# Kernel tuning notes

Hardware: AMD Instinct MI355X
Metric: run time of the kernel (lower is better)

The kernel has to match this reference:

```python
import jax, jax.numpy as jnp
import numpy as np
import math

B, Q_LEN, K_LEN = 8, 512, 512
D_MODEL, H = 512, 8
DK = D_MODEL // H


def setup_inputs() -> dict:
    key = jax.random.key(0)
    ks = jax.random.split(key, 12)
    inp = {
        "query": jax.random.normal(ks[0], (B, Q_LEN, D_MODEL), jnp.float32),
        "key": jax.random.normal(ks[1], (B, K_LEN, D_MODEL), jnp.float32),
        "value": jax.random.normal(ks[2], (B, K_LEN, D_MODEL), jnp.float32),
        "relative_embeddings": jax.random.normal(ks[3], (K_LEN, Q_LEN, D_MODEL), jnp.float32),
        # causal mask: 1 = attend, 0 = masked
        "mask": jnp.tril(jnp.ones((Q_LEN, K_LEN), dtype=bool)),
        "Wq": jax.random.normal(ks[4], (D_MODEL, D_MODEL), jnp.float32) / math.sqrt(D_MODEL),
        "Wk": jax.random.normal(ks[5], (D_MODEL, D_MODEL), jnp.float32) / math.sqrt(D_MODEL),
        "Wv": jax.random.normal(ks[6], (D_MODEL, D_MODEL), jnp.float32) / math.sqrt(D_MODEL),
        "Wo": jax.random.normal(ks[7], (D_MODEL, D_MODEL), jnp.float32) / math.sqrt(D_MODEL),
        "Wr": jax.random.normal(ks[8], (D_MODEL, D_MODEL), jnp.float32) / math.sqrt(D_MODEL),
        "u": jax.random.normal(ks[9], (H, DK), jnp.float32),
        "v": jax.random.normal(ks[10], (H, DK), jnp.float32),
    }
    return inp


def reference(query, key, value, relative_embeddings, mask, Wq, Wk, Wv, Wo, Wr, u, v):
    b, q_len, d_model = query.shape
    k_len = key.shape[1]
    # torch nn.Linear(x) = x @ W.T (bias=False)
    Qh = (query @ Wq.T).reshape(b, q_len, H, DK).transpose(0, 2, 1, 3)   # bhqd
    Kh = (key @ Wk.T).reshape(b, k_len, H, DK).transpose(0, 2, 1, 3)     # bhkd
    Vh = (value @ Wv.T).reshape(b, k_len, H, DK).transpose(0, 2, 1, 3)   # bhkd
    # relative position projection: (k_len, q_len, d_model)
    R = relative_embeddings @ Wr.T
    # view(k,q,H,dk).permute(2,1,0,3) -> (H, q, k, dk)
    Rh = R.reshape(k_len, q_len, H, DK).transpose(2, 1, 0, 3)
    # content score: (Q + u) K^T
    content = jnp.einsum("bhqd,bhkd->bhqk", Qh + u[None, :, None, :], Kh)
    # position score: (Q + v) R^T, R per-head per-query
    position = jnp.einsum("bhqd,hqkd->bhqk", Qh + v[None, :, None, :], Rh)
    scores = (content + position) / math.sqrt(DK)
    scores = jnp.where(mask[None, None, :, :], scores, -1e9)
    weights = jax.nn.softmax(scores, axis=-1)  # dropout is identity in eval
    out = jnp.einsum("bhqk,bhkd->bhqd", weights, Vh)
    out = out.transpose(0, 2, 1, 3).reshape(b, q_len, d_model)
    out = out @ Wo.T
    return (out, weights)
```

## Files before the change

### kernel.cpp

```cpp
#include <hip/hip_runtime.h>

#define BATCH   8
#define SEQ     512
#define DMODEL  512
#define NHEAD   8
#define DKH     64

typedef __attribute__((ext_vector_type(8))) short bf16x8;
typedef __attribute__((ext_vector_type(4))) float f32x4;

__device__ __forceinline__ short f2bf(float f) {
    union { float f; unsigned u; } v; v.f = f;
    unsigned r = v.u + 0x7FFFu + ((v.u >> 16) & 1u);
    return (short)(r >> 16);
}

#define LDK 40

__device__ __forceinline__ void stage_f32(const float* __restrict__ base,
                                          int rstride, short* lds, int tid) {
    int r = tid >> 2, c = (tid & 3) << 3;
    const float* p = base + (size_t)r * rstride + c;
    float4 x = *(const float4*)p;
    float4 y = *(const float4*)(p + 4);
    union { short s[8]; bf16x8 v; } o;
    o.s[0] = f2bf(x.x); o.s[1] = f2bf(x.y); o.s[2] = f2bf(x.z); o.s[3] = f2bf(x.w);
    o.s[4] = f2bf(y.x); o.s[5] = f2bf(y.y); o.s[6] = f2bf(y.z); o.s[7] = f2bf(y.w);
    *(bf16x8*)(lds + r * LDK + c) = o.v;
}

__device__ __forceinline__ void stage_bf16(const short* __restrict__ base,
                                           int rstride, short* lds, int tid) {
    int r = tid >> 2, c = (tid & 3) << 3;
    bf16x8 v = *(const bf16x8*)(base + (size_t)r * rstride + c);
    *(bf16x8*)(lds + r * LDK + c) = v;
}

__device__ __forceinline__ void mma_tile(const short* As, const short* Bs,
                                         int lane, int wm, int wn, f32x4 acc[2][2]) {
    int lo = lane & 15, hi = lane >> 4;
    bf16x8 a0 = *(const bf16x8*)(As + (wm * 32 + lo) * LDK + hi * 8);
    bf16x8 a1 = *(const bf16x8*)(As + (wm * 32 + 16 + lo) * LDK + hi * 8);
    bf16x8 b0 = *(const bf16x8*)(Bs + (wn * 32 + lo) * LDK + hi * 8);
    bf16x8 b1 = *(const bf16x8*)(Bs + (wn * 32 + 16 + lo) * LDK + hi * 8);
    acc[0][0] = __builtin_amdgcn_mfma_f32_16x16x32_bf16(a0, b0, acc[0][0], 0, 0, 0);
    acc[0][1] = __builtin_amdgcn_mfma_f32_16x16x32_bf16(a0, b1, acc[0][1], 0, 0, 0);
    acc[1][0] = __builtin_amdgcn_mfma_f32_16x16x32_bf16(a1, b0, acc[1][0], 0, 0, 0);
    acc[1][1] = __builtin_amdgcn_mfma_f32_16x16x32_bf16(a1, b1, acc[1][1], 0, 0, 0);
}

__global__ __launch_bounds__(256) void qkvw_kernel(
        const float* __restrict__ query, const float* __restrict__ key_,
        const float* __restrict__ value,
        const float* __restrict__ Wq, const float* __restrict__ Wk,
        const float* __restrict__ Wv, const float* __restrict__ Wr,
        const float* __restrict__ uvec, const float* __restrict__ vvec,
        short* __restrict__ Qu, short* __restrict__ Qv,
        short* __restrict__ Kh, short* __restrict__ Vt,
        short* __restrict__ Wrt) {
    __shared__ short As[64 * LDK], Bs[64 * LDK];
    int f = blockIdx.x, tid = threadIdx.x;
    if (f >= 1536) {
        int base = (f - 1536) * 1024;
        #pragma unroll
        for (int j = 0; j < 4; j++) {
            int idx = base + j * 256 + tid;
            int n = idx >> 9, m = idx & 511;
            Wrt[idx] = f2bf(Wr[(size_t)m * 512 + n]);
        }
        return;
    }
    int i = f >> 3;
    int nt = i & 7;
    int gm = (f & 7) * 24 + (i >> 3);
    int mode = gm >> 6, mt = gm & 63;
    const float* x = mode == 0 ? query : (mode == 1 ? key_ : value);
    const float* W = mode == 0 ? Wq : (mode == 1 ? Wk : Wv);
    int lane = tid & 63, w = tid >> 6, wm = w >> 1, wn = w & 1;
    const float* Abase = x + (size_t)mt * 64 * DMODEL;
    const float* Bbase = W + (size_t)nt * 64 * DMODEL;
    f32x4 acc[2][2] = {};
    for (int kt = 0; kt < DMODEL; kt += 32) {
        __syncthreads();
        stage_f32(Abase + kt, DMODEL, As, tid);
        stage_f32(Bbase + kt, DMODEL, Bs, tid);
        __syncthreads();
        mma_tile(As, Bs, lane, wm, wn, acc);
    }
    int lo = lane & 15, hi = lane >> 4;
    for (int fm = 0; fm < 2; fm++)
        for (int fn = 0; fn < 2; fn++)
            for (int r = 0; r < 4; r++) {
                int m = mt * 64 + wm * 32 + fm * 16 + hi * 4 + r;
                int n = nt * 64 + wn * 32 + fn * 16 + lo;
                float val = acc[fm][fn][r];
                int b = m >> 9, s = m & 511, h = n >> 6, d = n & 63;
                if (mode == 0) {
                    size_t idx = ((size_t)(b * NHEAD + h) * SEQ + s) * DKH + d;
                    Qu[idx] = f2bf(val + uvec[n]);
                    Qv[idx] = f2bf(val + vvec[n]);
                } else if (mode == 1) {
                    Kh[((size_t)(b * NHEAD + h) * SEQ + s) * DKH + d] = f2bf(val);
                } else {
                    Vt[((size_t)(b * NHEAD + h) * DKH + d) * SEQ + s] = f2bf(val);
                }
            }
}

__global__ __launch_bounds__(256) void t_kernel(const short* __restrict__ Qv,
                                                const short* __restrict__ Wrt,
                                                short* __restrict__ T2) {
    __shared__ short As[64 * LDK], Bs[64 * LDK];
    int f = blockIdx.x;
    int i = f >> 3;
    int nt = i & 7;
    int mh = (f & 7) * 64 + (i >> 3);
    int mt = mh >> 3, h = mh & 7;
    int tid = threadIdx.x, lane = tid & 63, w = tid >> 6, wm = w >> 1, wn = w & 1;
    int m0 = mt * 64, b = m0 >> 9, q0 = m0 & 511;
    const short* Abase = Qv + ((size_t)(b * NHEAD + h) * SEQ + q0) * DKH;
    const short* Bbase = Wrt + (size_t)nt * 64 * DMODEL + h * DKH;
    f32x4 acc[2][2] = {};
    for (int kt = 0; kt < DKH; kt += 32) {
        __syncthreads();
        stage_bf16(Abase + kt, DKH, As, tid);
        stage_bf16(Bbase + kt, DMODEL, Bs, tid);
        __syncthreads();
        mma_tile(As, Bs, lane, wm, wn, acc);
    }
    int lo = lane & 15, hi = lane >> 4;
    int bh = b * NHEAD + h;
    for (int fm = 0; fm < 2; fm++)
        for (int fn = 0; fn < 2; fn++)
            for (int r = 0; r < 4; r++) {
                int q = q0 + wm * 32 + fm * 16 + hi * 4 + r;
                int n = nt * 64 + wn * 32 + fn * 16 + lo;
                T2[((size_t)q * 64 + bh) * DMODEL + n] = f2bf(acc[fm][fn][r]);
            }
}

__global__ __launch_bounds__(256) void content_kernel(const short* __restrict__ Qu,
                                                      const short* __restrict__ Kh,
                                                      float* __restrict__ scores) {
    int f = blockIdx.x;
    int i = f >> 3;
    int bh = (f & 7) * 8 + (i >> 6);
    int rest = i & 63;
    int kt_ = rest & 7, qt = rest >> 3;
    if (kt_ > qt) return;
    __shared__ short As[64 * LDK], Bs[64 * LDK];
    int tid = threadIdx.x, lane = tid & 63, w = tid >> 6, wm = w >> 1, wn = w & 1;
    const short* Abase = Qu + ((size_t)bh * SEQ + qt * 64) * DKH;
    const short* Bbase = Kh + ((size_t)bh * SEQ + kt_ * 64) * DKH;
    f32x4 acc[2][2] = {};
    for (int kt = 0; kt < DKH; kt += 32) {
        __syncthreads();
        stage_bf16(Abase + kt, DKH, As, tid);
        stage_bf16(Bbase + kt, DKH, Bs, tid);
        __syncthreads();
        mma_tile(As, Bs, lane, wm, wn, acc);
    }
    int lo = lane & 15, hi = lane >> 4;
    for (int fm = 0; fm < 2; fm++)
        for (int fn = 0; fn < 2; fn++)
            for (int r = 0; r < 4; r++) {
                int q = qt * 64 + wm * 32 + fm * 16 + hi * 4 + r;
                int k = kt_ * 64 + wn * 32 + fn * 16 + lo;
                scores[((size_t)bh * SEQ + q) * SEQ + k] = acc[fm][fn][r];
            }
}

__global__ __launch_bounds__(512) void position_kernel(const short* __restrict__ T2,
                                                       const float* __restrict__ rel,
                                                       float* __restrict__ scores) {
    int bk = blockIdx.x;
    int x = bk & 7, idx = bk >> 3;
    int q = (idx >> 1) * 8 + x;
    int half = idx & 1;
    if (half * 256 > q) return;
    __shared__ short Tl[64 * 512];
    int tid = threadIdx.x, w = tid >> 6, lane = tid & 63;
    const short* Tq = T2 + (size_t)q * (64 * DMODEL);
    #pragma unroll
    for (int it = 0; it < 8; ++it) {
        int chunk = it * 512 + tid;
        int r = chunk >> 6, c = chunk & 63;
        bf16x8 v = *(const bf16x8*)(Tq + (size_t)chunk * 8);
        *(bf16x8*)(Tl + r * 512 + (c ^ (r & 7)) * 8) = v;
    }
    __syncthreads();
    int kbase = half * 256 + w * 32;
    if (kbase > q) return;
    int lo = lane & 15, hi = lane >> 4;
    const float* relq = rel + ((size_t)kbase * SEQ + q) * DMODEL;
    f32x4 acc[4][2] = {};
    for (int n = 0; n < DMODEL; n += 32) {
        bf16x8 a[4];
        #pragma unroll
        for (int fm = 0; fm < 4; fm++) {
            int rr = fm * 16 + lo;
            int g = ((n >> 3) + hi) ^ (rr & 7);
            a[fm] = *(const bf16x8*)(Tl + rr * 512 + g * 8);
        }
        bf16x8 bfrag[2];
        #pragma unroll
        for (int fk = 0; fk < 2; fk++) {
            const float* p = relq + (size_t)(fk * 16 + lo) * (SEQ * DMODEL) + n + hi * 8;
            float4 xv = *(const float4*)p;
            float4 yv = *(const float4*)(p + 4);
            union { short s[8]; bf16x8 v; } o;
            o.s[0] = f2bf(xv.x); o.s[1] = f2bf(xv.y); o.s[2] = f2bf(xv.z); o.s[3] = f2bf(xv.w);
            o.s[4] = f2bf(yv.x); o.s[5] = f2bf(yv.y); o.s[6] = f2bf(yv.z); o.s[7] = f2bf(yv.w);
            bfrag[fk] = o.v;
        }
        #pragma unroll
        for (int fm = 0; fm < 4; fm++) {
            acc[fm][0] = __builtin_amdgcn_mfma_f32_16x16x32_bf16(a[fm], bfrag[0], acc[fm][0], 0, 0, 0);
            acc[fm][1] = __builtin_amdgcn_mfma_f32_16x16x32_bf16(a[fm], bfrag[1], acc[fm][1], 0, 0, 0);
        }
    }
    #pragma unroll
    for (int fm = 0; fm < 4; fm++)
        #pragma unroll
        for (int fk = 0; fk < 2; fk++)
            #pragma unroll
            for (int r = 0; r < 4; r++) {
                int bh = fm * 16 + hi * 4 + r;
                int k = kbase + fk * 16 + lo;
                scores[((size_t)bh * SEQ + q) * SEQ + k] += acc[fm][fk][r];
            }
}

__global__ __launch_bounds__(256) void pv_sm_kernel(float* __restrict__ scores,
                                                    const short* __restrict__ Vt,
                                                    short* __restrict__ attn) {
    __shared__ short As[64 * LDK], Bs[64 * LDK];
    int f = blockIdx.x;
    int i = f >> 3;
    int bh = (f & 7) * 8 + (i >> 3);
    int qt = i & 7;
    int tid = threadIdx.x, lane = tid & 63, w = tid >> 6, wm = w >> 1, wn = w & 1;
    int kmax = (qt + 1) * 64;
    int r = tid >> 2, c4 = tid & 3;
    int q = qt * 64 + r;
    float* row = scores + ((size_t)bh * SEQ + q) * SEQ;
    float M = -1e30f, S = 0.f;
    int kbeg = c4 * 128;
    int kend = (kbeg + 128 < kmax) ? kbeg + 128 : kmax;
    for (int k = kbeg; k < kend; k += 4) {
        float4 vv = *(const float4*)(row + k);
        float x0 = (k + 0 <= q) ? vv.x * 0.125f : -1e30f;
        float x1 = (k + 1 <= q) ? vv.y * 0.125f : -1e30f;
        float x2 = (k + 2 <= q) ? vv.z * 0.125f : -1e30f;
        float x3 = (k + 3 <= q) ? vv.w * 0.125f : -1e30f;
        float mx = fmaxf(fmaxf(x0, x1), fmaxf(x2, x3));
        float Mn = fmaxf(M, mx);
        S = S * __expf(M - Mn) + __expf(x0 - Mn) + __expf(x1 - Mn)
          + __expf(x2 - Mn) + __expf(x3 - Mn);
        M = Mn;
    }
    #pragma unroll
    for (int off = 1; off <= 2; off <<= 1) {
        float Mo = __shfl_xor(M, off), So = __shfl_xor(S, off);
        float Mn = fmaxf(M, Mo);
        S = S * __expf(M - Mn) + So * __expf(Mo - Mn);
        M = Mn;
    }
    float invS = 1.0f / S;
    const short* Bbase = Vt + (size_t)bh * DKH * SEQ;
    f32x4 acc[2][2] = {};
    int cc = c4 * 8;
    for (int kt = 0; kt < SEQ; kt += 32) {
        if (kt < kmax) {
            __syncthreads();
            stage_bf16(Bbase + kt, SEQ, Bs, tid);
            float4 x = *(const float4*)(row + kt + cc);
            float4 y = *(const float4*)(row + kt + cc + 4);
            float p0 = (kt + cc + 0 <= q) ? __expf(x.x * 0.125f - M) * invS : 0.f;
            float p1 = (kt + cc + 1 <= q) ? __expf(x.y * 0.125f - M) * invS : 0.f;
            float p2 = (kt + cc + 2 <= q) ? __expf(x.z * 0.125f - M) * invS : 0.f;
            float p3 = (kt + cc + 3 <= q) ? __expf(x.w * 0.125f - M) * invS : 0.f;
            float p4 = (kt + cc + 4 <= q) ? __expf(y.x * 0.125f - M) * invS : 0.f;
            float p5 = (kt + cc + 5 <= q) ? __expf(y.y * 0.125f - M) * invS : 0.f;
            float p6 = (kt + cc + 6 <= q) ? __expf(y.z * 0.125f - M) * invS : 0.f;
            float p7 = (kt + cc + 7 <= q) ? __expf(y.w * 0.125f - M) * invS : 0.f;
            *(float4*)(row + kt + cc) = make_float4(p0, p1, p2, p3);
            *(float4*)(row + kt + cc + 4) = make_float4(p4, p5, p6, p7);
            union { short s[8]; bf16x8 v; } o;
            o.s[0] = f2bf(p0); o.s[1] = f2bf(p1); o.s[2] = f2bf(p2); o.s[3] = f2bf(p3);
            o.s[4] = f2bf(p4); o.s[5] = f2bf(p5); o.s[6] = f2bf(p6); o.s[7] = f2bf(p7);
            *(bf16x8*)(As + r * LDK + cc) = o.v;
            __syncthreads();
            mma_tile(As, Bs, lane, wm, wn, acc);
        } else {
            float4 z = make_float4(0.f, 0.f, 0.f, 0.f);
            *(float4*)(row + kt + cc) = z;
            *(float4*)(row + kt + cc + 4) = z;
        }
    }
    int lo = lane & 15, hi = lane >> 4;
    int b = bh >> 3, h = bh & 7;
    for (int fm = 0; fm < 2; fm++)
        for (int fn = 0; fn < 2; fn++)
            for (int rr = 0; rr < 4; rr++) {
                int qq = qt * 64 + wm * 32 + fm * 16 + hi * 4 + rr;
                int d = wn * 32 + fn * 16 + lo;
                attn[((size_t)b * SEQ + qq) * DMODEL + h * DKH + d] = f2bf(acc[fm][fn][rr]);
            }
}

__global__ __launch_bounds__(256) void oproj_kernel(const short* __restrict__ attn,
                                                    const float* __restrict__ Wo,
                                                    float* __restrict__ out) {
    __shared__ short As[64 * LDK], Bs[64 * LDK];
    int f = blockIdx.x;
    int i = f >> 3;
    int mt = (f & 7) * 8 + (i >> 3);
    int nt = i & 7;
    int tid = threadIdx.x, lane = tid & 63, w = tid >> 6, wm = w >> 1, wn = w & 1;
    const short* Abase = attn + (size_t)mt * 64 * DMODEL;
    const float* Bbase = Wo + (size_t)nt * 64 * DMODEL;
    f32x4 acc[2][2] = {};
    for (int kt = 0; kt < DMODEL; kt += 32) {
        __syncthreads();
        stage_bf16(Abase + kt, DMODEL, As, tid);
        stage_f32(Bbase + kt, DMODEL, Bs, tid);
        __syncthreads();
        mma_tile(As, Bs, lane, wm, wn, acc);
    }
    int lo = lane & 15, hi = lane >> 4;
    for (int fm = 0; fm < 2; fm++)
        for (int fn = 0; fn < 2; fn++)
            for (int r = 0; r < 4; r++) {
                int m = mt * 64 + wm * 32 + fm * 16 + hi * 4 + r;
                int n = nt * 64 + wn * 32 + fn * 16 + lo;
                out[(size_t)m * DMODEL + n] = acc[fm][fn][r];
            }
}

extern "C" void kernel_launch(void* const* d_in, const int* in_sizes, int n_in,
                              void* d_out, int out_size, void* d_ws, size_t ws_size,
                              hipStream_t stream) {
    (void)in_sizes; (void)n_in; (void)out_size; (void)ws_size;
    const float* query = (const float*)d_in[0];
    const float* key   = (const float*)d_in[1];
    const float* value = (const float*)d_in[2];
    const float* rel   = (const float*)d_in[3];
    const float* Wq = (const float*)d_in[5];
    const float* Wk = (const float*)d_in[6];
    const float* Wv = (const float*)d_in[7];
    const float* Wo = (const float*)d_in[8];
    const float* Wr = (const float*)d_in[9];
    const float* u  = (const float*)d_in[10];
    const float* v  = (const float*)d_in[11];

    float* out     = (float*)d_out;
    float* weights = out + (size_t)BATCH * SEQ * DMODEL;

    char* ws = (char*)d_ws;
    short* Qu   = (short*)(ws);
    short* Qv   = (short*)(ws + ((size_t)4 << 20));
    short* Kh   = (short*)(ws + ((size_t)8 << 20));
    short* Vt   = (short*)(ws + ((size_t)12 << 20));
    short* T2   = (short*)(ws + ((size_t)16 << 20));
    short* attn = (short*)(ws + ((size_t)48 << 20));
    short* Wrt  = (short*)(ws + ((size_t)52 << 20));

    qkvw_kernel<<<1792, 256, 0, stream>>>(query, key, value, Wq, Wk, Wv, Wr,
                                          u, v, Qu, Qv, Kh, Vt, Wrt);
    t_kernel<<<4096, 256, 0, stream>>>(Qv, Wrt, T2);
    content_kernel<<<4096, 256, 0, stream>>>(Qu, Kh, weights);
    position_kernel<<<1024, 512, 0, stream>>>(T2, rel, weights);
    pv_sm_kernel<<<512, 256, 0, stream>>>(weights, Vt, attn);
    oproj_kernel<<<512, 256, 0, stream>>>(attn, Wo, out);
}
```

Before: 215.5 us.

## Merge T and content kernels; single-pass softmax with P cached in LDS

Measured after the change: 201.8 us. 6.4% less time.

```diff
diff --git a/kernel.cpp b/kernel.cpp
--- a/kernel.cpp
+++ b/kernel.cpp
@@ -13,6 +13,10 @@
     union { float f; unsigned u; } v; v.f = f;
     unsigned r = v.u + 0x7FFFu + ((v.u >> 16) & 1u);
     return (short)(r >> 16);
+}
+__device__ __forceinline__ float bf2f(short s) {
+    union { unsigned u; float f; } v; v.u = ((unsigned)(unsigned short)s) << 16;
+    return v.f;
 }
 
 #define LDK 40
@@ -107,67 +111,66 @@
             }
 }
 
-__global__ __launch_bounds__(256) void t_kernel(const short* __restrict__ Qv,
-                                                const short* __restrict__ Wrt,
-                                                short* __restrict__ T2) {
+__global__ __launch_bounds__(256) void tc_kernel(const short* __restrict__ Qv,
+                                                 const short* __restrict__ Wrt,
+                                                 short* __restrict__ T2,
+                                                 const short* __restrict__ Qu,
+                                                 const short* __restrict__ Kh,
+                                                 float* __restrict__ scores) {
     __shared__ short As[64 * LDK], Bs[64 * LDK];
-    int f = blockIdx.x;
-    int i = f >> 3;
-    int nt = i & 7;
-    int mh = (f & 7) * 64 + (i >> 3);
-    int mt = mh >> 3, h = mh & 7;
-    int tid = threadIdx.x, lane = tid & 63, w = tid >> 6, wm = w >> 1, wn = w & 1;
-    int m0 = mt * 64, b = m0 >> 9, q0 = m0 & 511;
-    const short* Abase = Qv + ((size_t)(b * NHEAD + h) * SEQ + q0) * DKH;
-    const short* Bbase = Wrt + (size_t)nt * 64 * DMODEL + h * DKH;
-    f32x4 acc[2][2] = {};
-    for (int kt = 0; kt < DKH; kt += 32) {
-        __syncthreads();
-        stage_bf16(Abase + kt, DKH, As, tid);
-        stage_bf16(Bbase + kt, DMODEL, Bs, tid);
-        __syncthreads();
-        mma_tile(As, Bs, lane, wm, wn, acc);
-    }
-    int lo = lane & 15, hi = lane >> 4;
-    int bh = b * NHEAD + h;
-    for (int fm = 0; fm < 2; fm++)
-        for (int fn = 0; fn < 2; fn++)
-            for (int r = 0; r < 4; r++) {
-                int q = q0 + wm * 32 + fm * 16 + hi * 4 + r;
-                int n = nt * 64 + wn * 32 + fn * 16 + lo;
-                T2[((size_t)q * 64 + bh) * DMODEL + n] = f2bf(acc[fm][fn][r]);
-            }
-}
-
-__global__ __launch_bounds__(256) void content_kernel(const short* __restrict__ Qu,
-                                                      const short* __restrict__ Kh,
-                                                      float* __restrict__ scores) {
-    int f = blockIdx.x;
-    int i = f >> 3;
-    int bh = (f & 7) * 8 + (i >> 6);
-    int rest = i & 63;
-    int kt_ = rest & 7, qt = rest >> 3;
-    if (kt_ > qt) return;
-    __shared__ short As[64 * LDK], Bs[64 * LDK];
-    int tid = threadIdx.x, lane = tid & 63, w = tid >> 6, wm = w >> 1, wn = w & 1;
-    const short* Abase = Qu + ((size_t)bh * SEQ + qt * 64) * DKH;
-    const short* Bbase = Kh + ((size_t)bh * SEQ + kt_ * 64) * DKH;
-    f32x4 acc[2][2] = {};
-    for (int kt = 0; kt < DKH; kt += 32) {
-        __syncthreads();
-        stage_bf16(Abase + kt, DKH, As, tid);
-        stage_bf16(Bbase + kt, DKH, Bs, tid);
-        __syncthreads();
-        mma_tile(As, Bs, lane, wm, wn, acc);
-    }
-    int lo = lane & 15, hi = lane >> 4;
-    for (int fm = 0; fm < 2; fm++)
-        for (int fn = 0; fn < 2; fn++)
-            for (int r = 0; r < 4; r++) {
-                int q = qt * 64 + wm * 32 + fm * 16 + hi * 4 + r;
-                int k = kt_ * 64 + wn * 32 + fn * 16 + lo;
-                scores[((size_t)bh * SEQ + q) * SEQ + k] = acc[fm][fn][r];
-            }
+    int f0 = blockIdx.x, tid = threadIdx.x;
+    int lane = tid & 63, w = tid >> 6, wm = w >> 1, wn = w & 1;
+    int lo = lane & 15, hi = lane >> 4;
+    if (f0 < 4096) {
+        int f = f0;
+        int i = f >> 3;
+        int nt = i & 7;
+        int mh = (f & 7) * 64 + (i >> 3);
+        int mt = mh >> 3, h = mh & 7;
+        int m0 = mt * 64, b = m0 >> 9, q0 = m0 & 511;
+        const short* Abase = Qv + ((size_t)(b * NHEAD + h) * SEQ + q0) * DKH;
+        const short* Bbase = Wrt + (size_t)nt * 64 * DMODEL + h * DKH;
+        f32x4 acc[2][2] = {};
+        for (int kt = 0; kt < DKH; kt += 32) {
+            __syncthreads();
+            stage_bf16(Abase + kt, DKH, As, tid);
+            stage_bf16(Bbase + kt, DMODEL, Bs, tid);
+            __syncthreads();
+            mma_tile(As, Bs, lane, wm, wn, acc);
+        }
+        int bh = b * NHEAD + h;
+        for (int fm = 0; fm < 2; fm++)
+            for (int fn = 0; fn < 2; fn++)
+                for (int r = 0; r < 4; r++) {
+                    int q = q0 + wm * 32 + fm * 16 + hi * 4 + r;
+                    int n = nt * 64 + wn * 32 + fn * 16 + lo;
+                    T2[((size_t)q * 64 + bh) * DMODEL + n] = f2bf(acc[fm][fn][r]);
+                }
+    } else {
+        int f = f0 - 4096;
+        int i = f >> 3;
+        int bh = (f & 7) * 8 + (i >> 6);
+        int rest = i & 63;
+        int kt_ = rest & 7, qt = rest >> 3;
+        if (kt_ > qt) return;
+        const short* Abase = Qu + ((size_t)bh * SEQ + qt * 64) * DKH;
+        const short* Bbase = Kh + ((size_t)bh * SEQ + kt_ * 64) * DKH;
+        f32x4 acc[2][2] = {};
+        for (int kt = 0; kt < DKH; kt += 32) {
+            __syncthreads();
+            stage_bf16(Abase + kt, DKH, As, tid);
+            stage_bf16(Bbase + kt, DKH, Bs, tid);
+            __syncthreads();
+            mma_tile(As, Bs, lane, wm, wn, acc);
+        }
+        for (int fm = 0; fm < 2; fm++)
+            for (int fn = 0; fn < 2; fn++)
+                for (int r = 0; r < 4; r++) {
+                    int q = qt * 64 + wm * 32 + fm * 16 + hi * 4 + r;
+                    int k = kt_ * 64 + wn * 32 + fn * 16 + lo;
+                    scores[((size_t)bh * SEQ + q) * SEQ + k] = acc[fm][fn][r];
+                }
+    }
 }
 
 __global__ __launch_bounds__(512) void position_kernel(const short* __restrict__ T2,
@@ -231,10 +234,13 @@
             }
 }
 
+#define PSTR 520
 __global__ __launch_bounds__(256) void pv_sm_kernel(float* __restrict__ scores,
                                                     const short* __restrict__ Vt,
                                                     short* __restrict__ attn) {
-    __shared__ short As[64 * LDK], Bs[64 * LDK];
+    __shared__ short Ps[64 * PSTR];
+    __shared__ short Bs[64 * LDK];
+    __shared__ float invS_lds[64];
     int f = blockIdx.x;
     int i = f >> 3;
     int bh = (f & 7) * 8 + (i >> 3);
@@ -243,69 +249,67 @@
     int kmax = (qt + 1) * 64;
     int r = tid >> 2, c4 = tid & 3;
     int q = qt * 64 + r;
+    int cc = c4 * 8;
     float* row = scores + ((size_t)bh * SEQ + q) * SEQ;
-    float M = -1e30f, S = 0.f;
-    int kbeg = c4 * 128;
-    int kend = (kbeg + 128 < kmax) ? kbeg + 128 : kmax;
-    for (int k = kbeg; k < kend; k += 4) {
-        float4 vv = *(const float4*)(row + k);
-        float x0 = (k + 0 <= q) ? vv.x * 0.125f : -1e30f;
-        float x1 = (k + 1 <= q) ? vv.y * 0.125f : -1e30f;
-        float x2 = (k + 2 <= q) ? vv.z * 0.125f : -1e30f;
-        float x3 = (k + 3 <= q) ? vv.w * 0.125f : -1e30f;
-        float mx = fmaxf(fmaxf(x0, x1), fmaxf(x2, x3));
-        float Mn = fmaxf(M, mx);
-        S = S * __expf(M - Mn) + __expf(x0 - Mn) + __expf(x1 - Mn)
-          + __expf(x2 - Mn) + __expf(x3 - Mn);
-        M = Mn;
-    }
-    #pragma unroll
-    for (int off = 1; off <= 2; off <<= 1) {
-        float Mo = __shfl_xor(M, off), So = __shfl_xor(S, off);
-        float Mn = fmaxf(M, Mo);
-        S = S * __expf(M - Mn) + So * __expf(Mo - Mn);
-        M = Mn;
-    }
+    float S = 0.f;
+    for (int kt = 0; kt < kmax; kt += 32) {
+        float4 x = *(const float4*)(row + kt + cc);
+        float4 y = *(const float4*)(row + kt + cc + 4);
+        float p0 = (kt + cc + 0 <= q) ? __expf(x.x * 0.125f) : 0.f;
+        float p1 = (kt + cc + 1 <= q) ? __expf(x.y * 0.125f) : 0.f;
+        float p2 = (kt + cc + 2 <= q) ? __expf(x.z * 0.125f) : 0.f;
+        float p3 = (kt + cc + 3 <= q) ? __expf(x.w * 0.125f) : 0.f;
+        float p4 = (kt + cc + 4 <= q) ? __expf(y.x * 0.125f) : 0.f;
+        float p5 = (kt + cc + 5 <= q) ? __expf(y.y * 0.125f) : 0.f;
+        float p6 = (kt + cc + 6 <= q) ? __expf(y.z * 0.125f) : 0.f;
+        float p7 = (kt + cc + 7 <= q) ? __expf(y.w * 0.125f) : 0.f;
+        S += p0 + p1 + p2 + p3 + p4 + p5 + p6 + p7;
+        union { short s[8]; bf16x8 v; } o;
+        o.s[0] = f2bf(p0); o.s[1] = f2bf(p1); o.s[2] = f2bf(p2); o.s[3] = f2bf(p3);
+        o.s[4] = f2bf(p4); o.s[5] = f2bf(p5); o.s[6] = f2bf(p6); o.s[7] = f2bf(p7);
+        *(bf16x8*)(Ps + r * PSTR + kt + cc) = o.v;
+    }
+    S += __shfl_xor(S, 1); S += __shfl_xor(S, 2);
     float invS = 1.0f / S;
+    if (c4 == 0) invS_lds[r] = invS;
+    for (int kt = 0; kt < SEQ; kt += 32) {
+        float4 o0, o1;
+        if (kt < kmax) {
+            const short* pr = Ps + r * PSTR + kt + cc;
+            o0 = make_float4(bf2f(pr[0]) * invS, bf2f(pr[1]) * invS,
+                             bf2f(pr[2]) * invS, bf2f(pr[3]) * invS);
+            o1 = make_float4(bf2f(pr[4]) * invS, bf2f(pr[5]) * invS,
+                             bf2f(pr[6]) * invS, bf2f(pr[7]) * invS);
+        } else {
+            o0 = make_float4(0.f, 0.f, 0.f, 0.f); o1 = o0;
+        }
+        *(float4*)(row + kt + cc) = o0;
+        *(float4*)(row + kt + cc + 4) = o1;
+    }
     const short* Bbase = Vt + (size_t)bh * DKH * SEQ;
+    int lo = lane & 15, hi = lane >> 4;
     f32x4 acc[2][2] = {};
-    int cc = c4 * 8;
-    for (int kt = 0; kt < SEQ; kt += 32) {
-        if (kt < kmax) {
-            __syncthreads();
-            stage_bf16(Bbase + kt, SEQ, Bs, tid);
-            float4 x = *(const float4*)(row + kt + cc);
-            float4 y = *(const float4*)(row + kt + cc + 4);
-            float p0 = (kt + cc + 0 <= q) ? __expf(x.x * 0.125f - M) * invS : 0.f;
-            float p1 = (kt + cc + 1 <= q) ? __expf(x.y * 0.125f - M) * invS : 0.f;
-            float p2 = (kt + cc + 2 <= q) ? __expf(x.z * 0.125f - M) * invS : 0.f;
-            float p3 = (kt + cc + 3 <= q) ? __expf(x.w * 0.125f - M) * invS : 0.f;
-            float p4 = (kt + cc + 4 <= q) ? __expf(y.x * 0.125f - M) * invS : 0.f;
-            float p5 = (kt + cc + 5 <= q) ? __expf(y.y * 0.125f - M) * invS : 0.f;
-            float p6 = (kt + cc + 6 <= q) ? __expf(y.z * 0.125f - M) * invS : 0.f;
-            float p7 = (kt + cc + 7 <= q) ? __expf(y.w * 0.125f - M) * invS : 0.f;
-            *(float4*)(row + kt + cc) = make_float4(p0, p1, p2, p3);
-            *(float4*)(row + kt + cc + 4) = make_float4(p4, p5, p6, p7);
-            union { short s[8]; bf16x8 v; } o;
-            o.s[0] = f2bf(p0); o.s[1] = f2bf(p1); o.s[2] = f2bf(p2); o.s[3] = f2bf(p3);
-            o.s[4] = f2bf(p4); o.s[5] = f2bf(p5); o.s[6] = f2bf(p6); o.s[7] = f2bf(p7);
-            *(bf16x8*)(As + r * LDK + cc) = o.v;
-            __syncthreads();
-            mma_tile(As, Bs, lane, wm, wn, acc);
-        } else {
-            float4 z = make_float4(0.f, 0.f, 0.f, 0.f);
-            *(float4*)(row + kt + cc) = z;
-            *(float4*)(row + kt + cc + 4) = z;
-        }
-    }
-    int lo = lane & 15, hi = lane >> 4;
+    for (int kc = 0; kc < kmax; kc += 32) {
+        __syncthreads();
+        stage_bf16(Bbase + kc, SEQ, Bs, tid);
+        __syncthreads();
+        bf16x8 a0 = *(const bf16x8*)(Ps + (wm * 32 + lo) * PSTR + kc + hi * 8);
+        bf16x8 a1 = *(const bf16x8*)(Ps + (wm * 32 + 16 + lo) * PSTR + kc + hi * 8);
+        bf16x8 b0 = *(const bf16x8*)(Bs + (wn * 32 + lo) * LDK + hi * 8);
+        bf16x8 b1 = *(const bf16x8*)(Bs + (wn * 32 + 16 + lo) * LDK + hi * 8);
+        acc[0][0] = __builtin_amdgcn_mfma_f32_16x16x32_bf16(a0, b0, acc[0][0], 0, 0, 0);
+        acc[0][1] = __builtin_amdgcn_mfma_f32_16x16x32_bf16(a0, b1, acc[0][1], 0, 0, 0);
+        acc[1][0] = __builtin_amdgcn_mfma_f32_16x16x32_bf16(a1, b0, acc[1][0], 0, 0, 0);
+        acc[1][1] = __builtin_amdgcn_mfma_f32_16x16x32_bf16(a1, b1, acc[1][1], 0, 0, 0);
+    }
     int b = bh >> 3, h = bh & 7;
     for (int fm = 0; fm < 2; fm++)
         for (int fn = 0; fn < 2; fn++)
             for (int rr = 0; rr < 4; rr++) {
-                int qq = qt * 64 + wm * 32 + fm * 16 + hi * 4 + rr;
+                int ql = wm * 32 + fm * 16 + hi * 4 + rr;
                 int d = wn * 32 + fn * 16 + lo;
-                attn[((size_t)b * SEQ + qq) * DMODEL + h * DKH + d] = f2bf(acc[fm][fn][rr]);
+                float val = acc[fm][fn][rr] * invS_lds[ql];
+                attn[((size_t)b * SEQ + qt * 64 + ql) * DMODEL + h * DKH + d] = f2bf(val);
             }
 }
 
@@ -368,8 +372,7 @@
 
     qkvw_kernel<<<1792, 256, 0, stream>>>(query, key, value, Wq, Wk, Wv, Wr,
                                           u, v, Qu, Qv, Kh, Vt, Wrt);
-    t_kernel<<<4096, 256, 0, stream>>>(Qv, Wrt, T2);
-    content_kernel<<<4096, 256, 0, stream>>>(Qu, Kh, weights);
+    tc_kernel<<<8192, 256, 0, stream>>>(Qv, Wrt, T2, Qu, Kh, weights);
     position_kernel<<<1024, 512, 0, stream>>>(T2, rel, weights);
     pv_sm_kernel<<<512, 256, 0, stream>>>(weights, Vt, attn);
     oproj_kernel<<<512, 256, 0, stream>>>(attn, Wo, out);
```
